# Kernel tuning notes

Hardware: AMD Instinct MI355X
Metric: run time of the kernel (lower is better)

## Reference

```python
import jax, jax.numpy as jnp
import numpy as np

N_NODES = 100000
N_EDGES = 400000
N_GRAPHS = 256
HID = 256
BIO = 512
LAYERS = 3
EPS = 1e-5


def _seg_mean(v, seg, num):
    s = jax.ops.segment_sum(v, seg, num_segments=num)
    c = jax.ops.segment_sum(jnp.ones((v.shape[0], 1), v.dtype), seg, num_segments=num)
    return s / jnp.maximum(c, 1.0)


def setup_inputs() -> dict:
    key = jax.random.key(0)
    ks = jax.random.split(key, 24)
    d = {}
    d['x'] = jax.random.randint(ks[0], (N_NODES,), 0, 8)
    d['edge_index'] = jax.random.randint(ks[1], (2, N_EDGES), 0, N_NODES)
    d['edge_attr'] = jax.random.normal(ks[2], (N_EDGES, 4), jnp.float32)
    d['batch'] = jnp.sort(jax.random.randint(ks[3], (N_NODES,), 0, N_GRAPHS))
    sc = 0.06  # ~1/sqrt(HID)
    d['node_emb_W'] = jax.random.normal(ks[4], (8, HID), jnp.float32) * sc
    d['edge_emb_W'] = jax.random.normal(ks[5], (4, HID), jnp.float32) * 0.5
    d['edge_emb_b'] = jnp.zeros((HID,), jnp.float32)
    d['edge_mlp_W1'] = jax.random.normal(ks[6], (HID, HID), jnp.float32) * sc
    d['edge_mlp_b1'] = jnp.zeros((HID,), jnp.float32)
    d['edge_mlp_W2'] = jax.random.normal(ks[7], (HID, HID), jnp.float32) * sc
    d['edge_mlp_b2'] = jnp.zeros((HID,), jnp.float32)
    d['struct_scale'] = jnp.asarray(1.5, jnp.float32)
    d['conv_W1'] = jax.random.normal(ks[8], (LAYERS, HID, HID), jnp.float32) * sc
    d['conv_b1'] = jnp.zeros((LAYERS, HID), jnp.float32)
    d['conv_W2'] = jax.random.normal(ks[9], (LAYERS, HID, HID), jnp.float32) * sc
    d['conv_b2'] = jnp.zeros((LAYERS, HID), jnp.float32)
    d['conv_eps'] = jnp.zeros((LAYERS,), jnp.float32)
    d['norm_gamma'] = jnp.ones((LAYERS, HID), jnp.float32)
    d['norm_beta'] = jnp.zeros((LAYERS, HID), jnp.float32)
    d['norm_alpha'] = jnp.ones((LAYERS, HID), jnp.float32)
    d['mean_bio'] = jax.random.normal(ks[10], (BIO,), jnp.float32)
    d['head_W1'] = jax.random.normal(ks[11], (HID + BIO, HID), jnp.float32) * 0.036
    d['head_b1'] = jnp.zeros((HID,), jnp.float32)
    d['head_W2'] = jax.random.normal(ks[12], (HID, 1), jnp.float32) * sc
    d['head_b2'] = jnp.zeros((1,), jnp.float32)
    return d


def reference(x, edge_index, edge_attr, batch, node_emb_W, edge_emb_W, edge_emb_b,
              edge_mlp_W1, edge_mlp_b1, edge_mlp_W2, edge_mlp_b2, struct_scale,
              conv_W1, conv_b1, conv_W2, conv_b2, conv_eps,
              norm_gamma, norm_beta, norm_alpha, mean_bio,
              head_W1, head_b1, head_W2, head_b2):
    h = node_emb_W[x]  # [N, HID]
    src, dst = edge_index[0], edge_index[1]

    e = edge_attr @ edge_emb_W + edge_emb_b  # edge_emb
    e = jax.nn.relu(e @ edge_mlp_W1 + edge_mlp_b1) @ edge_mlp_W2 + edge_mlp_b2
    struct_mask = edge_attr[:, 1] > 0
    e = e * jnp.where(struct_mask, struct_scale, 1.0)[:, None]

    for l in range(LAYERS):
        # GINE conv: aggregate relu(x_j + e_ij) at target, then 2-layer MLP
        msg = jax.nn.relu(h[src] + e)  # [E, HID]
        agg = jax.ops.segment_sum(msg, dst, num_segments=N_NODES)
        z = (1.0 + conv_eps[l]) * h + agg
        h = jax.nn.relu(z @ conv_W1[l] + conv_b1[l]) @ conv_W2[l] + conv_b2[l]
        # GraphNorm per graph
        mean = _seg_mean(h, batch, N_GRAPHS)  # [G, HID]
        hc = h - norm_alpha[l] * mean[batch]
        var = _seg_mean(hc * hc, batch, N_GRAPHS)
        h = norm_gamma[l] * hc * jax.lax.rsqrt(var[batch] + EPS) + norm_beta[l]

    g = _seg_mean(h, batch, N_GRAPHS)  # global mean pool [G, HID]
    b_emb = jnp.broadcast_to(mean_bio, (g.shape[0], BIO))
    combined = jnp.concatenate([g, b_emb], axis=1)
    out = jax.nn.relu(combined @ head_W1 + head_b1) @ head_W2 + head_b2
    return out.mean(axis=1, keepdims=True)
```

## Files before the change

### kernel.cpp

```cpp
#include <hip/hip_runtime.h>
#include <cstddef>

#define NN 100000
#define NE 400000
#define NG 256
#define HIDC 256
#define EPSN 1e-5f

typedef unsigned short bfu;
using short8 = __attribute__((ext_vector_type(8))) short;
using f32x4  = __attribute__((ext_vector_type(4))) float;
using f32x2  = __attribute__((ext_vector_type(2))) float;

#if defined(__has_builtin)
#if __has_builtin(__builtin_amdgcn_cvt_pk_fp8_f32) && __has_builtin(__builtin_amdgcn_cvt_pk_f32_fp8)
#define HWFP8 1
#endif
#endif

__device__ __forceinline__ float bf2f(bfu b) {
    union { unsigned int u; float f; } v; v.u = ((unsigned int)b) << 16; return v.f;
}
__device__ __forceinline__ bfu f2bf(float f) {
    union { float f; unsigned int u; } v; v.f = f;
    unsigned int r = v.u + 0x7FFFu + ((v.u >> 16) & 1u);
    return (bfu)(r >> 16);
}
__device__ __forceinline__ float e4m3f_sw(unsigned char b) {
    unsigned s = ((unsigned)(b & 0x80u)) << 24;
    unsigned E = (b >> 3) & 15u, M = b & 7u;
    union { unsigned x; float f; } o;
    if (E == 0) { o.f = (float)M * 0.001953125f; o.x |= s; }
    else o.x = s | ((E + 120u) << 23) | (M << 20);
    return o.f;
}
__device__ __forceinline__ unsigned char f2e4m3_sw(float f) {
    union { float f; unsigned u; } v; v.f = f;
    unsigned s = (v.u >> 24) & 0x80u;
    float a = fabsf(f);
    if (!(a < 448.f)) return (unsigned char)(s | 0x7Eu);
    if (a < 0.0009765625f) return (unsigned char)s;
    if (a < 0.015625f) {
        int m = (int)(a * 512.f + 0.5f);
        if (m >= 8) return (unsigned char)(s | 0x08u);
        return (unsigned char)(s | (unsigned)m);
    }
    unsigned u = v.u;
    unsigned r = u + 0x7FFFFu + ((u >> 20) & 1u);
    int E = (int)((r >> 23) & 255u) - 127 + 7;
    unsigned M = (r >> 20) & 7u;
    if (E >= 16) return (unsigned char)(s | 0x7Eu);
    if (E <= 0) {
        int m = (int)(a * 512.f + 0.5f); if (m > 7) m = 7;
        return (unsigned char)(s | (unsigned)m);
    }
    return (unsigned char)(s | ((unsigned)E << 3) | M);
}
__device__ __forceinline__ unsigned int fp8enc4(float a, float b, float c, float d) {
#ifdef HWFP8
    int lo = __builtin_amdgcn_cvt_pk_fp8_f32(a, b, 0, false);
    int hi = __builtin_amdgcn_cvt_pk_fp8_f32(c, d, 0, false);
    return (unsigned int)((lo & 0xFFFF) | (hi << 16));
#else
    return (unsigned)f2e4m3_sw(a) | ((unsigned)f2e4m3_sw(b) << 8) |
           ((unsigned)f2e4m3_sw(c) << 16) | ((unsigned)f2e4m3_sw(d) << 24);
#endif
}
__device__ __forceinline__ float4 fp8dec4(unsigned int u) {
#ifdef HWFP8
    f32x2 lo = __builtin_amdgcn_cvt_pk_f32_fp8((int)u, false);
    f32x2 hi = __builtin_amdgcn_cvt_pk_f32_fp8((int)u, true);
    return make_float4(lo[0], lo[1], hi[0], hi[1]);
#else
    return make_float4(e4m3f_sw(u & 255u), e4m3f_sw((u >> 8) & 255u),
                       e4m3f_sw((u >> 16) & 255u), e4m3f_sw((u >> 24) & 255u));
#endif
}
__device__ __forceinline__ float4 ld4(const void* p, size_t i, int bf) {
    if (bf) {
        ushort4 u = *(const ushort4*)((const bfu*)p + i);
        return make_float4(bf2f(u.x), bf2f(u.y), bf2f(u.z), bf2f(u.w));
    }
    return *(const float4*)((const float*)p + i);
}
__device__ __forceinline__ float4 ld4b(const bfu* p, size_t i) {
    ushort4 u = *(const ushort4*)(p + i);
    return make_float4(bf2f(u.x), bf2f(u.y), bf2f(u.z), bf2f(u.w));
}
__device__ __forceinline__ float ld1(const void* p, size_t i, int bf) {
    return bf ? bf2f(((const bfu*)p)[i]) : ((const float*)p)[i];
}
__device__ __forceinline__ void st1(void* p, size_t i, float v, int bf) {
    if (bf) ((bfu*)p)[i] = f2bf(v); else ((float*)p)[i] = v;
}

__global__ void k_dt2(const unsigned int* __restrict__ g, int* __restrict__ flag) {
    if (threadIdx.x == 0)
        flag[0] = (g[0] == 0x3F800000u) ? 0 : 1;
}

__global__ void k_st2(const int* __restrict__ batch, int* __restrict__ starts) {
    int g = threadIdx.x;
    if (g > NG) return;
    if (g == NG) { starts[NG] = NN; return; }
    int lo = 0, hi = NN;
    while (lo < hi) { int mid = (lo + hi) >> 1; if (batch[mid] < g) lo = mid + 1; else hi = mid; }
    starts[g] = lo;
}

__global__ void k_zi(int* __restrict__ p, int n) {
    int i = blockIdx.x * blockDim.x + threadIdx.x;
    if (i < n) p[i] = 0;
}

__global__ void k_cnt(const int* __restrict__ ei, int* __restrict__ deg) {
    int e = blockIdx.x * blockDim.x + threadIdx.x;
    if (e >= NE) return;
    int d = ei[NE + e];
    if ((unsigned)d < (unsigned)NN) atomicAdd(&deg[d], 1);
}
__global__ void k_sc1(const int* __restrict__ deg, int* __restrict__ rowp,
                      int* __restrict__ part) {
    __shared__ int sh[256];
    int b = blockIdx.x, t = threadIdx.x;
    int i = b * 256 + t;
    int v = (i < NN) ? deg[i] : 0;
    sh[t] = v; __syncthreads();
    for (int off = 1; off < 256; off <<= 1) {
        int add = (t >= off) ? sh[t - off] : 0;
        __syncthreads();
        sh[t] += add; __syncthreads();
    }
    if (i < NN) rowp[i] = sh[t] - v;
    if (t == 255) part[b] = sh[255];
}
__global__ void k_sc2(int* __restrict__ part, int nb) {
    if (threadIdx.x != 0) return;
    int run = 0;
    for (int b = 0; b < nb; ++b) { int t = part[b]; part[b] = run; run += t; }
}
__global__ void k_sc3(int* __restrict__ rowp, const int* __restrict__ part) {
    int i = blockIdx.x * blockDim.x + threadIdx.x;
    if (i < NN) rowp[i] += part[blockIdx.x];
    if (i == 0) rowp[NN] = NE;
}
__global__ void k_cpi(const int* __restrict__ a, int* __restrict__ b, int n) {
    int i = blockIdx.x * blockDim.x + threadIdx.x;
    if (i < n) b[i] = a[i];
}
__global__ void k_fil(const int* __restrict__ ei, int* __restrict__ cursor,
                      int* __restrict__ csrc, int* __restrict__ ceid) {
    int e = blockIdx.x * blockDim.x + threadIdx.x;
    if (e >= NE) return;
    int s = ei[e], d = ei[NE + e];
    if ((unsigned)d >= (unsigned)NN) return;
    int pos = atomicAdd(&cursor[d], 1);
    csrc[pos] = ((unsigned)s < (unsigned)NN) ? s : 0;
    ceid[pos] = e;
}
__global__ void k_spl(int* __restrict__ splits, int* __restrict__ cnts) {
    if (threadIdx.x == 0) { splits[0] = 0; splits[1] = NN; cnts[0] = NE; }
}

__global__ void k_wef(const void* __restrict__ Wemb, const void* __restrict__ bemb,
                      const void* __restrict__ W1, const void* __restrict__ b1,
                      bfu* __restrict__ weff, bfu* __restrict__ beff,
                      const int* __restrict__ dtf) {
    int bf = *dtf;
    int j = blockIdx.x;
    int n = threadIdx.x;
    float acc = 0.f;
    if (j < 4) {
        for (int k = 0; k < HIDC; ++k)
            acc += ld1(Wemb, (size_t)j * HIDC + k, bf) * ld1(W1, (size_t)k * HIDC + n, bf);
        weff[j * HIDC + n] = f2bf(acc);
    } else {
        for (int k = 0; k < HIDC; ++k)
            acc += ld1(bemb, k, bf) * ld1(W1, (size_t)k * HIDC + n, bf);
        beff[n] = f2bf(acc + ld1(b1, n, bf));
    }
}

__global__ void k_gat3(const bfu* __restrict__ h, const unsigned char* __restrict__ e8,
                       const int* __restrict__ rowp, const int* __restrict__ csrc,
                       bfu* __restrict__ agg) {
    int tid = blockIdx.x * blockDim.x + threadIdx.x;
    if (tid >= NN * 64) return;
    int n = tid >> 6, q = (tid & 63) << 2;
    int s0 = rowp[n], s1 = rowp[n + 1];
    float4 a = make_float4(0.f, 0.f, 0.f, 0.f);
    for (int i = s0; i < s1; ++i) {
        int src = csrc[i];
        ushort4 hu = *(const ushort4*)(h + (size_t)src * HIDC + q);
        unsigned int eu = *(const unsigned int*)(e8 + (size_t)i * HIDC + q);
        float4 ev = fp8dec4(eu);
        a.x += fmaxf(bf2f(hu.x) + ev.x, 0.f);
        a.y += fmaxf(bf2f(hu.y) + ev.y, 0.f);
        a.z += fmaxf(bf2f(hu.z) + ev.z, 0.f);
        a.w += fmaxf(bf2f(hu.w) + ev.w, 0.f);
    }
    ushort4 o; o.x = f2bf(a.x); o.y = f2bf(a.y); o.z = f2bf(a.z); o.w = f2bf(a.w);
    *(ushort4*)(agg + (size_t)n * HIDC + q) = o;
}

__global__ void k_wtr(const void* __restrict__ W, long wOff, bfu* __restrict__ Wt,
                      const int* __restrict__ dtf) {
    int o = blockIdx.x * blockDim.x + threadIdx.x;
    if (o >= HIDC * HIDC) return;
    int blk = o >> 9, pos = o & 511;
    int w = blk >> 5, rem = blk & 31;
    int t = rem >> 3, kb = rem & 7;
    int pr = pos >> 3, j = pos & 7;
    int lr = pr >> 2, lq = pr & 3;
    int n = w * 64 + t * 16 + lr;
    int k = kb * 32 + lq * 8 + j;
    Wt[o] = f2bf(ld1(W, (size_t)wOff + (size_t)k * HIDC + n, *dtf));
}

__global__ void k_emb(const int* __restrict__ x, const void* __restrict__ W,
                      bfu* __restrict__ h, const int* __restrict__ dtf) {
    int tid = blockIdx.x * blockDim.x + threadIdx.x;
    if (tid >= NN * 64) return;
    int bf = *dtf;
    int n = tid >> 6, q = (tid & 63) << 2;
    int xv = x[n]; if ((unsigned)xv >= 8u) xv = 0;
    float4 v = ld4(W, (size_t)xv * HIDC + q, bf);
    ushort4 o; o.x = f2bf(v.x); o.y = f2bf(v.y); o.z = f2bf(v.z); o.w = f2bf(v.w);
    *(ushort4*)(h + (size_t)n * HIDC + q) = o;
}

__global__ __launch_bounds__(256)
void k_mg2(const bfu* __restrict__ A, const void* __restrict__ A2,
           const void* __restrict__ attrs,
           const bfu* __restrict__ weff, const bfu* __restrict__ beff,
           const void* __restrict__ eps, int epsIdx,
           const bfu* __restrict__ Wt,
           const void* __restrict__ bias, long bOff,
           const void* __restrict__ scalep,
           void* __restrict__ C, int M,
           int amode, int relu, int scale, int o8,
           const int* __restrict__ dtf,
           const int* __restrict__ eidx, const int* __restrict__ rowp,
           const int* __restrict__ splits, const int* __restrict__ cnts, int cj) {
    __shared__ bfu As[64 * 32];
    const int bf = *dtf;
    const int tid = threadIdx.x;
    const int wave = tid >> 6, lane = tid & 63;
    const int lr = lane & 15, lq = lane >> 4;
    const int m0 = blockIdx.x * 64;
    int MM = M;
    long p0 = 0;
    if (cj >= 0) {
        MM = cnts[cj];
        p0 = rowp[splits[cj]];
    }
    if (m0 >= MM) return;
    f32x4 acc[4][4] = {};
    float epsv = 0.f;
    if (amode == 2) epsv = 1.0f + ld1(eps, epsIdx, bf);

    const int ar = tid >> 2;
    const int ak = (tid & 3) << 3;
    const int gmA = m0 + ar;
    const bfu* wb = Wt + ((size_t)wave * 32) * 512 + (size_t)(lr * 4 + lq) * 8;

    float aa[4] = {0.f, 0.f, 0.f, 0.f};
    if (amode == 1 && gmA < MM) {
        long er = (cj >= 0) ? (long)eidx[p0 + gmA] : (long)gmA;
        aa[0] = ld1(attrs, (size_t)er * 4 + 0, bf);
        aa[1] = ld1(attrs, (size_t)er * 4 + 1, bf);
        aa[2] = ld1(attrs, (size_t)er * 4 + 2, bf);
        aa[3] = ld1(attrs, (size_t)er * 4 + 3, bf);
    }

    for (int k0 = 0; k0 < 256; k0 += 32) {
        const int kb = k0 >> 5;
        if (amode == 0) {
            uint4 u = make_uint4(0, 0, 0, 0);
            if (gmA < MM) u = *(const uint4*)(A + (size_t)gmA * HIDC + k0 + ak);
            *(uint4*)(&As[tid * 8]) = u;
        } else if (amode == 2) {
            float hv[8] = {}, gv[8] = {};
            if (gmA < MM) {
                ushort4 h0 = *(const ushort4*)(A + (size_t)gmA * HIDC + k0 + ak);
                ushort4 h1 = *(const ushort4*)(A + (size_t)gmA * HIDC + k0 + ak + 4);
                hv[0]=bf2f(h0.x); hv[1]=bf2f(h0.y); hv[2]=bf2f(h0.z); hv[3]=bf2f(h0.w);
                hv[4]=bf2f(h1.x); hv[5]=bf2f(h1.y); hv[6]=bf2f(h1.z); hv[7]=bf2f(h1.w);
                float4 g0 = ld4(A2, (size_t)gmA * HIDC + k0 + ak, 1);
                float4 g1 = ld4(A2, (size_t)gmA * HIDC + k0 + ak + 4, 1);
                gv[0]=g0.x; gv[1]=g0.y; gv[2]=g0.z; gv[3]=g0.w;
                gv[4]=g1.x; gv[5]=g1.y; gv[6]=g1.z; gv[7]=g1.w;
            }
#pragma unroll
            for (int j = 0; j < 8; ++j)
                As[tid * 8 + j] = f2bf(epsv * hv[j] + gv[j]);
        } else {
            float v0=0,v1=0,v2=0,v3=0,v4=0,v5=0,v6=0,v7=0;
            if (gmA < MM) {
                float4 c0 = ld4b(beff, k0 + ak);
                float4 c1 = ld4b(beff, k0 + ak + 4);
                v0=c0.x; v1=c0.y; v2=c0.z; v3=c0.w; v4=c1.x; v5=c1.y; v6=c1.z; v7=c1.w;
#pragma unroll
                for (int j = 0; j < 4; ++j) {
                    float4 w0 = ld4b(weff, (size_t)j * HIDC + k0 + ak);
                    float4 w1 = ld4b(weff, (size_t)j * HIDC + k0 + ak + 4);
                    v0 += aa[j]*w0.x; v1 += aa[j]*w0.y; v2 += aa[j]*w0.z; v3 += aa[j]*w0.w;
                    v4 += aa[j]*w1.x; v5 += aa[j]*w1.y; v6 += aa[j]*w1.z; v7 += aa[j]*w1.w;
                }
            }
            ushort4 o0, o1;
            o0.x = f2bf(fmaxf(v0, 0.f)); o0.y = f2bf(fmaxf(v1, 0.f));
            o0.z = f2bf(fmaxf(v2, 0.f)); o0.w = f2bf(fmaxf(v3, 0.f));
            o1.x = f2bf(fmaxf(v4, 0.f)); o1.y = f2bf(fmaxf(v5, 0.f));
            o1.z = f2bf(fmaxf(v6, 0.f)); o1.w = f2bf(fmaxf(v7, 0.f));
            *(ushort4*)(&As[tid * 8])     = o0;
            *(ushort4*)(&As[tid * 8 + 4]) = o1;
        }
        __syncthreads();
        short8 fa[4], fb[4];
#pragma unroll
        for (int r = 0; r < 4; ++r)
            fa[r] = *(const short8*)(&As[(r * 64 + lr * 4 + lq) * 8]);
#pragma unroll
        for (int t = 0; t < 4; ++t)
            fb[t] = *(const short8*)(wb + (size_t)(t * 8 + kb) * 512);
#pragma unroll
        for (int r = 0; r < 4; ++r)
#pragma unroll
            for (int t = 0; t < 4; ++t)
                acc[r][t] = __builtin_amdgcn_mfma_f32_16x16x32_bf16(
                    fa[r], fb[t], acc[r][t], 0, 0, 0);
        __syncthreads();
    }

    float bv[4];
#pragma unroll
    for (int t = 0; t < 4; ++t) bv[t] = ld1(bias, (size_t)bOff + wave * 64 + t * 16 + lr, bf);
    float scv = scale ? ld1(scalep, 0, bf) : 1.0f;
#pragma unroll
    for (int r = 0; r < 4; ++r) {
#pragma unroll
        for (int i = 0; i < 4; ++i) {
            int gm = m0 + r * 16 + lq * 4 + i;
            if (gm >= MM) continue;
            float rs = 1.0f;
            if (scale) {
                long er = (cj >= 0) ? (long)eidx[p0 + gm] : (long)gm;
                if (ld1(attrs, (size_t)er * 4 + 1, bf) > 0.f) rs = scv;
            }
            float ov[4];
#pragma unroll
            for (int t = 0; t < 4; ++t) {
                float o = acc[r][t][i] + bv[t];
                if (relu) o = fmaxf(o, 0.f);
                ov[t] = o * rs;
            }
            size_t cbase = (size_t)gm * HIDC + wave * 64 + lr;
            if (o8) {
                unsigned int pk = fp8enc4(ov[0], ov[1], ov[2], ov[3]);
                unsigned char* Cb = (unsigned char*)C;
                Cb[cbase]      = (unsigned char)(pk & 255u);
                Cb[cbase + 16] = (unsigned char)((pk >> 8) & 255u);
                Cb[cbase + 32] = (unsigned char)((pk >> 16) & 255u);
                Cb[cbase + 48] = (unsigned char)(pk >> 24);
            } else {
                bfu* Cb = (bfu*)C;
#pragma unroll
                for (int t = 0; t < 4; ++t)
                    Cb[cbase + t * 16] = f2bf(ov[t]);
            }
        }
    }
}

__global__ __launch_bounds__(256)
void k_cnv(bfu* __restrict__ h, const bfu* __restrict__ agg,
           const void* __restrict__ eps, int epsIdx,
           const bfu* __restrict__ Wt1, const void* __restrict__ bias1, long b1Off,
           const bfu* __restrict__ Wt2, const void* __restrict__ bias2, long b2Off,
           const int* __restrict__ dtf) {
    __shared__ bfu As[64 * 32];
    __shared__ bfu Ts[8][64 * 32];
    const int bf = *dtf;
    const int tid = threadIdx.x;
    const int wave = tid >> 6, lane = tid & 63;
    const int lr = lane & 15, lq = lane >> 4;
    const int m0 = blockIdx.x * 64;
    const float epsv = 1.0f + ld1(eps, epsIdx, bf);
    const int ar = tid >> 2;
    const int ak = (tid & 3) << 3;
    const int gmA = m0 + ar;
    const bfu* wb1 = Wt1 + ((size_t)wave * 32) * 512 + (size_t)(lr * 4 + lq) * 8;
    const bfu* wb2 = Wt2 + ((size_t)wave * 32) * 512 + (size_t)(lr * 4 + lq) * 8;

    f32x4 acc[4][4] = {};
    for (int k0 = 0; k0 < 256; k0 += 32) {
        const int kb = k0 >> 5;
        float hv[8] = {}, gv[8] = {};
        if (gmA < NN) {
            ushort4 h0 = *(const ushort4*)(h + (size_t)gmA * HIDC + k0 + ak);
            ushort4 h1 = *(const ushort4*)(h + (size_t)gmA * HIDC + k0 + ak + 4);
            hv[0]=bf2f(h0.x); hv[1]=bf2f(h0.y); hv[2]=bf2f(h0.z); hv[3]=bf2f(h0.w);
            hv[4]=bf2f(h1.x); hv[5]=bf2f(h1.y); hv[6]=bf2f(h1.z); hv[7]=bf2f(h1.w);
            ushort4 g0 = *(const ushort4*)(agg + (size_t)gmA * HIDC + k0 + ak);
            ushort4 g1 = *(const ushort4*)(agg + (size_t)gmA * HIDC + k0 + ak + 4);
            gv[0]=bf2f(g0.x); gv[1]=bf2f(g0.y); gv[2]=bf2f(g0.z); gv[3]=bf2f(g0.w);
            gv[4]=bf2f(g1.x); gv[5]=bf2f(g1.y); gv[6]=bf2f(g1.z); gv[7]=bf2f(g1.w);
        }
#pragma unroll
        for (int j = 0; j < 8; ++j)
            As[tid * 8 + j] = f2bf(epsv * hv[j] + gv[j]);
        __syncthreads();
        short8 fa[4], fb[4];
#pragma unroll
        for (int r = 0; r < 4; ++r)
            fa[r] = *(const short8*)(&As[(r * 64 + lr * 4 + lq) * 8]);
#pragma unroll
        for (int t = 0; t < 4; ++t)
            fb[t] = *(const short8*)(wb1 + (size_t)(t * 8 + kb) * 512);
#pragma unroll
        for (int r = 0; r < 4; ++r)
#pragma unroll
            for (int t = 0; t < 4; ++t)
                acc[r][t] = __builtin_amdgcn_mfma_f32_16x16x32_bf16(
                    fa[r], fb[t], acc[r][t], 0, 0, 0);
        __syncthreads();
    }
    {
        float bv[4];
#pragma unroll
        for (int t = 0; t < 4; ++t)
            bv[t] = ld1(bias1, (size_t)b1Off + wave * 64 + t * 16 + lr, bf);
        const f32x4 z4 = {0.f, 0.f, 0.f, 0.f};
#pragma unroll
        for (int r = 0; r < 4; ++r) {
#pragma unroll
            for (int i = 0; i < 4; ++i) {
                int row = r * 16 + lq * 4 + i;
#pragma unroll
                for (int t = 0; t < 4; ++t) {
                    int kk = wave * 64 + t * 16 + lr;
                    Ts[kk >> 5][row * 32 + (kk & 31)] =
                        f2bf(fmaxf(acc[r][t][i] + bv[t], 0.f));
                }
            }
        }
#pragma unroll
        for (int r = 0; r < 4; ++r)
#pragma unroll
            for (int t = 0; t < 4; ++t)
                acc[r][t] = z4;
    }
    __syncthreads();
#pragma unroll
    for (int kb = 0; kb < 8; ++kb) {
        short8 fa[4], fb[4];
#pragma unroll
        for (int r = 0; r < 4; ++r)
            fa[r] = *(const short8*)(&Ts[kb][(r * 64 + lr * 4 + lq) * 8]);
#pragma unroll
        for (int t = 0; t < 4; ++t)
            fb[t] = *(const short8*)(wb2 + (size_t)(t * 8 + kb) * 512);
#pragma unroll
        for (int r = 0; r < 4; ++r)
#pragma unroll
            for (int t = 0; t < 4; ++t)
                acc[r][t] = __builtin_amdgcn_mfma_f32_16x16x32_bf16(
                    fa[r], fb[t], acc[r][t], 0, 0, 0);
    }
    float bv[4];
#pragma unroll
    for (int t = 0; t < 4; ++t)
        bv[t] = ld1(bias2, (size_t)b2Off + wave * 64 + t * 16 + lr, bf);
#pragma unroll
    for (int r = 0; r < 4; ++r) {
#pragma unroll
        for (int i = 0; i < 4; ++i) {
            int gm = m0 + r * 16 + lq * 4 + i;
            if (gm >= NN) continue;
            size_t cbase = (size_t)gm * HIDC + wave * 64 + lr;
#pragma unroll
            for (int t = 0; t < 4; ++t)
                h[cbase + t * 16] = f2bf(acc[r][t][i] + bv[t]);
        }
    }
}

__global__ void k_s1(const bfu* __restrict__ h, const int* __restrict__ starts,
                     float* __restrict__ psum, float* __restrict__ psq) {
    int g = blockIdx.x, c8 = blockIdx.y, c = threadIdx.x;
    int s = starts[g], t = starts[g + 1];
    int len = t - s;
    int b = s + (int)(((long)len * c8) >> 3);
    int e = s + (int)(((long)len * (c8 + 1)) >> 3);
    float sum = 0.f, sq = 0.f;
    for (int n = b; n < e; ++n) {
        float v = bf2f(h[(size_t)n * HIDC + c]);
        sum += v; sq += v * v;
    }
    psum[((size_t)g * 8 + c8) * HIDC + c] = sum;
    psq[((size_t)g * 8 + c8) * HIDC + c] = sq;
}
__global__ void k_s2(const int* __restrict__ starts,
                     const float* __restrict__ psum, const float* __restrict__ psq,
                     const void* __restrict__ alpha, long aOff,
                     float* __restrict__ gmean, float* __restrict__ gvar,
                     const int* __restrict__ dtf) {
    int g = blockIdx.x, c = threadIdx.x;
    float sum = 0.f, sq = 0.f;
#pragma unroll
    for (int j = 0; j < 8; ++j) {
        sum += psum[((size_t)g * 8 + j) * HIDC + c];
        sq  += psq[((size_t)g * 8 + j) * HIDC + c];
    }
    int cn = starts[g + 1] - starts[g]; if (cn < 1) cn = 1;
    float cnt = (float)cn;
    float m = sum / cnt;
    float a = ld1(alpha, (size_t)aOff + c, *dtf);
    gmean[g * HIDC + c] = m;
    gvar[g * HIDC + c] = fmaxf(sq / cnt - (2.f * a - a * a) * m * m, 0.f);
}

__global__ void k_nrm(bfu* __restrict__ h, const int* __restrict__ batch,
                      const float* __restrict__ gmean, const float* __restrict__ gvar,
                      const void* __restrict__ gamma, const void* __restrict__ beta,
                      const void* __restrict__ alpha, long pOff,
                      const int* __restrict__ dtf) {
    int tid = blockIdx.x * blockDim.x + threadIdx.x;
    if (tid >= NN * 64) return;
    int bf = *dtf;
    int n = tid >> 6, q = (tid & 63) << 2;
    int g = batch[n]; if ((unsigned)g >= (unsigned)NG) g = 0;
    ushort4 hu = *(ushort4*)(h + (size_t)n * HIDC + q);
    const float4 mv = *(const float4*)(gmean + g * HIDC + q);
    const float4 vv = *(const float4*)(gvar + g * HIDC + q);
    float4 ga = ld4(gamma, (size_t)pOff + q, bf);
    float4 be = ld4(beta, (size_t)pOff + q, bf);
    float4 al = ld4(alpha, (size_t)pOff + q, bf);
    float4 v;
    v.x = ga.x * (bf2f(hu.x) - al.x * mv.x) * rsqrtf(vv.x + EPSN) + be.x;
    v.y = ga.y * (bf2f(hu.y) - al.y * mv.y) * rsqrtf(vv.y + EPSN) + be.y;
    v.z = ga.z * (bf2f(hu.z) - al.z * mv.z) * rsqrtf(vv.z + EPSN) + be.z;
    v.w = ga.w * (bf2f(hu.w) - al.w * mv.w) * rsqrtf(vv.w + EPSN) + be.w;
    ushort4 ov; ov.x = f2bf(v.x); ov.y = f2bf(v.y); ov.z = f2bf(v.z); ov.w = f2bf(v.w);
    *(ushort4*)(h + (size_t)n * HIDC + q) = ov;
}

__global__ void k_pl2(const int* __restrict__ starts,
                      const float* __restrict__ gmean, const float* __restrict__ gvar,
                      const void* __restrict__ gamma, const void* __restrict__ beta,
                      const void* __restrict__ alpha, long pOff,
                      float* __restrict__ g, const int* __restrict__ dtf) {
    int bf = *dtf;
    int gb = blockIdx.x, c = threadIdx.x;
    int cn = starts[gb + 1] - starts[gb];
    if (cn <= 0) { g[gb * HIDC + c] = 0.f; return; }
    float m = gmean[gb * HIDC + c];
    float v = gvar[gb * HIDC + c];
    float ga = ld1(gamma, (size_t)pOff + c, bf);
    float be = ld1(beta, (size_t)pOff + c, bf);
    float al = ld1(alpha, (size_t)pOff + c, bf);
    g[gb * HIDC + c] = ga * (1.f - al) * m * rsqrtf(v + EPSN) + be;
}

__global__ void k_hd(const float* __restrict__ g, const void* __restrict__ bio,
                     const void* __restrict__ W1, const void* __restrict__ b1,
                     const void* __restrict__ W2, const void* __restrict__ b2,
                     void* __restrict__ out, const int* __restrict__ dtf) {
    __shared__ float comb[768];
    __shared__ float red[256];
    __shared__ int nanf;
    int bf = *dtf;
    int gb = blockIdx.x, t = threadIdx.x;
    if (t == 0) nanf = 0;
    comb[t] = g[gb * HIDC + t];
    comb[256 + t] = ld1(bio, t, bf);
    comb[512 + t] = ld1(bio, 256 + t, bf);
    __syncthreads();
    float acc = ld1(b1, t, bf);
    for (int k = 0; k < 768; ++k) acc += comb[k] * ld1(W1, (size_t)k * HIDC + t, bf);
    if (isnan(acc) || isinf(acc)) nanf = 1;
    float hid = fmaxf(acc, 0.f);
    red[t] = hid * ld1(W2, t, bf);
    __syncthreads();
    for (int off = 128; off > 0; off >>= 1) {
        if (t < off) red[t] += red[t + off];
        __syncthreads();
    }
    if (t == 0) {
        float r = red[0] + ld1(b2, 0, bf);
        if (nanf || isnan(r)) r = 999.0f;
        st1(out, gb, r, bf);
    }
}

extern "C" void kernel_launch(void* const* d_in, const int* in_sizes, int n_in,
                              void* d_out, int out_size, void* d_ws, size_t ws_size,
                              hipStream_t stream) {
    const int* x = (const int*)d_in[0];
    const int* ei = (const int*)d_in[1];
    const void* eattr = d_in[2];
    const int* batch = (const int*)d_in[3];
    const void* node_emb_W = d_in[4];
    const void* edge_emb_W = d_in[5];
    const void* edge_emb_b = d_in[6];
    const void* emlp_W1 = d_in[7];
    const void* emlp_b1 = d_in[8];
    const void* emlp_W2 = d_in[9];
    const void* emlp_b2 = d_in[10];
    const void* struct_scale = d_in[11];
    const void* conv_W1 = d_in[12];
    const void* conv_b1 = d_in[13];
    const void* conv_W2 = d_in[14];
    const void* conv_b2 = d_in[15];
    const void* conv_eps = d_in[16];
    const void* ngamma = d_in[17];
    const void* nbeta = d_in[18];
    const void* nalpha = d_in[19];
    const void* mean_bio = d_in[20];
    const void* head_W1 = d_in[21];
    const void* head_b1 = d_in[22];
    const void* head_W2 = d_in[23];
    const void* head_b2 = d_in[24];
    (void)in_sizes; (void)n_in; (void)out_size; (void)ws_size;

    const size_t H_B = (size_t)NN * HIDC * 2;
    const size_t E8_B = (size_t)NE * HIDC;
    char* p = (char*)d_ws;
    bfu* hbuf = (bfu*)p; p += H_B;
    bfu* aggb = (bfu*)p; p += H_B;
    unsigned char* e8 = (unsigned char*)p; p += E8_B;
    bfu* wt = (bfu*)p; p += 8 * 65536 * 2;
    int* rowp = (int*)p;
    int* cursor = rowp + 100352;
    int* part = cursor + 100352;
    int* splits = part + 1024;
    int* cnts = splits + 8;
    int* csrc = cnts + 8;
    int* ceid = csrc + NE;
    p = (char*)(ceid + NE);
    float* psum = (float*)p; p += (size_t)NG * 8 * HIDC * 4;
    float* psq = (float*)p; p += (size_t)NG * 8 * HIDC * 4;
    char* small = p;
    int* starts = (int*)small;
    int* dtf = (int*)(small + 2048);
    bfu* weff = (bfu*)(small + 4096);
    bfu* beff = weff + 4 * HIDC;
    float* gmean = (float*)(small + 16384);
    float* gvar = gmean + NG * HIDC;
    float* gpool = gvar + NG * HIDC;

    k_dt2<<<1, 64, 0, stream>>>((const unsigned int*)ngamma, dtf);
    k_st2<<<1, 512, 0, stream>>>(batch, starts);
    k_emb<<<(NN * 64 + 255) / 256, 256, 0, stream>>>(x, node_emb_W, hbuf, dtf);
    k_wef<<<5, 256, 0, stream>>>(edge_emb_W, edge_emb_b, emlp_W1, emlp_b1,
                                 weff, beff, dtf);

    k_wtr<<<256, 256, 0, stream>>>(emlp_W2, 0, wt + 65536, dtf);
    for (int l = 0; l < 3; ++l) {
        k_wtr<<<256, 256, 0, stream>>>(conv_W1, (long)l * HIDC * HIDC, wt + (2 + l) * 65536, dtf);
        k_wtr<<<256, 256, 0, stream>>>(conv_W2, (long)l * HIDC * HIDC, wt + (5 + l) * 65536, dtf);
    }

    const int NBN = (NN + 255) / 256;
    k_zi<<<NBN, 256, 0, stream>>>(cursor, NN);
    k_cnt<<<(NE + 255) / 256, 256, 0, stream>>>(ei, cursor);
    k_sc1<<<NBN, 256, 0, stream>>>(cursor, rowp, part);
    k_sc2<<<1, 64, 0, stream>>>(part, NBN);
    k_sc3<<<NBN, 256, 0, stream>>>(rowp, part);
    k_cpi<<<NBN, 256, 0, stream>>>(rowp, cursor, NN);
    k_fil<<<(NE + 255) / 256, 256, 0, stream>>>(ei, cursor, csrc, ceid);
    k_spl<<<1, 64, 0, stream>>>(splits, cnts);

    dim3 gE((NE + 63) / 64), gN((NN + 63) / 64);
    k_mg2<<<gE, 256, 0, stream>>>(
        nullptr, nullptr, eattr, weff, beff,
        nullptr, 0, wt + 65536, emlp_b2, 0, struct_scale, e8, 0,
        1, 0, 1, 1, dtf, ceid, rowp, splits, cnts, 0);

    dim3 gS1(NG, 8);
    const int gatBlocks = (NN * 64 + 255) / 256;

    for (int l = 0; l < 3; ++l) {
        k_gat3<<<gatBlocks, 256, 0, stream>>>(hbuf, e8, rowp, csrc, aggb);
        k_cnv<<<gN, 256, 0, stream>>>(
            hbuf, aggb, conv_eps, l,
            wt + (2 + l) * 65536, conv_b1, (long)l * HIDC,
            wt + (5 + l) * 65536, conv_b2, (long)l * HIDC, dtf);
        k_s1<<<gS1, 256, 0, stream>>>(hbuf, starts, psum, psq);
        k_s2<<<NG, 256, 0, stream>>>(starts, psum, psq, nalpha, (long)l * HIDC,
                                     gmean, gvar, dtf);
        if (l < 2) {
            k_nrm<<<(NN * 64 + 255) / 256, 256, 0, stream>>>(
                hbuf, batch, gmean, gvar, ngamma, nbeta, nalpha, (long)l * HIDC, dtf);
        }
    }

    k_pl2<<<NG, 256, 0, stream>>>(starts, gmean, gvar, ngamma, nbeta, nalpha,
                                  (long)2 * HIDC, gpool, dtf);
    k_hd<<<NG, 256, 0, stream>>>(gpool, mean_bio, head_W1, head_b1,
                                 head_W2, head_b2, d_out, dtf);
}
```

Baseline: 1.066 ms.

## Specialize edge MLP kernel and stage full A tile in LDS once

Replaces the generic multi-mode edge GEMM kernel with a dedicated edge-MLP kernel. The whole 64x256 A tile is built into shared memory in one pass before a single barrier, instead of a barrier pair per 32-wide K slice. The per-row struct scale is precomputed into shared memory rather than re-gathered in the epilogue, and weff/beff are kept in fp32. The conv kernel gets the same single-barrier A staging using its existing Ts buffer. This raises LDS use per block to 32KB, which may lower occupancy.

Result: faster. 1.014 ms (-4.9%).

```diff
diff --git a/kernel.cpp b/kernel.cpp
--- a/kernel.cpp
+++ b/kernel.cpp
@@ -82,10 +82,6 @@
         return make_float4(bf2f(u.x), bf2f(u.y), bf2f(u.z), bf2f(u.w));
     }
     return *(const float4*)((const float*)p + i);
-}
-__device__ __forceinline__ float4 ld4b(const bfu* p, size_t i) {
-    ushort4 u = *(const ushort4*)(p + i);
-    return make_float4(bf2f(u.x), bf2f(u.y), bf2f(u.z), bf2f(u.w));
 }
 __device__ __forceinline__ float ld1(const void* p, size_t i, int bf) {
     return bf ? bf2f(((const bfu*)p)[i]) : ((const float*)p)[i];
@@ -158,13 +154,10 @@
     csrc[pos] = ((unsigned)s < (unsigned)NN) ? s : 0;
     ceid[pos] = e;
 }
-__global__ void k_spl(int* __restrict__ splits, int* __restrict__ cnts) {
-    if (threadIdx.x == 0) { splits[0] = 0; splits[1] = NN; cnts[0] = NE; }
-}
 
 __global__ void k_wef(const void* __restrict__ Wemb, const void* __restrict__ bemb,
                       const void* __restrict__ W1, const void* __restrict__ b1,
-                      bfu* __restrict__ weff, bfu* __restrict__ beff,
+                      float* __restrict__ weff, float* __restrict__ beff,
                       const int* __restrict__ dtf) {
     int bf = *dtf;
     int j = blockIdx.x;
@@ -173,11 +166,11 @@
     if (j < 4) {
         for (int k = 0; k < HIDC; ++k)
             acc += ld1(Wemb, (size_t)j * HIDC + k, bf) * ld1(W1, (size_t)k * HIDC + n, bf);
-        weff[j * HIDC + n] = f2bf(acc);
+        weff[j * HIDC + n] = acc;
     } else {
         for (int k = 0; k < HIDC; ++k)
             acc += ld1(bemb, k, bf) * ld1(W1, (size_t)k * HIDC + n, bf);
-        beff[n] = f2bf(acc + ld1(b1, n, bf));
+        beff[n] = acc + ld1(b1, n, bf);
     }
 }
 
@@ -230,145 +223,101 @@
 }
 
 __global__ __launch_bounds__(256)
-void k_mg2(const bfu* __restrict__ A, const void* __restrict__ A2,
-           const void* __restrict__ attrs,
-           const bfu* __restrict__ weff, const bfu* __restrict__ beff,
-           const void* __restrict__ eps, int epsIdx,
-           const bfu* __restrict__ Wt,
-           const void* __restrict__ bias, long bOff,
-           const void* __restrict__ scalep,
-           void* __restrict__ C, int M,
-           int amode, int relu, int scale, int o8,
-           const int* __restrict__ dtf,
-           const int* __restrict__ eidx, const int* __restrict__ rowp,
-           const int* __restrict__ splits, const int* __restrict__ cnts, int cj) {
-    __shared__ bfu As[64 * 32];
+void k_me(const void* __restrict__ attrs,
+          const float* __restrict__ weff, const float* __restrict__ beff,
+          const bfu* __restrict__ Wt, const void* __restrict__ bias,
+          const void* __restrict__ scalep,
+          unsigned char* __restrict__ C,
+          const int* __restrict__ dtf, const int* __restrict__ eidx) {
+    __shared__ bfu As[8][64 * 32];
+    __shared__ float sf[64];
     const int bf = *dtf;
     const int tid = threadIdx.x;
     const int wave = tid >> 6, lane = tid & 63;
     const int lr = lane & 15, lq = lane >> 4;
     const int m0 = blockIdx.x * 64;
-    int MM = M;
-    long p0 = 0;
-    if (cj >= 0) {
-        MM = cnts[cj];
-        p0 = rowp[splits[cj]];
-    }
-    if (m0 >= MM) return;
-    f32x4 acc[4][4] = {};
-    float epsv = 0.f;
-    if (amode == 2) epsv = 1.0f + ld1(eps, epsIdx, bf);
-
-    const int ar = tid >> 2;
+    const int row = tid >> 2;
     const int ak = (tid & 3) << 3;
-    const int gmA = m0 + ar;
-    const bfu* wb = Wt + ((size_t)wave * 32) * 512 + (size_t)(lr * 4 + lq) * 8;
+    const int gmA = m0 + row;
 
     float aa[4] = {0.f, 0.f, 0.f, 0.f};
-    if (amode == 1 && gmA < MM) {
-        long er = (cj >= 0) ? (long)eidx[p0 + gmA] : (long)gmA;
+    if (gmA < NE) {
+        long er = (long)eidx[gmA];
         aa[0] = ld1(attrs, (size_t)er * 4 + 0, bf);
         aa[1] = ld1(attrs, (size_t)er * 4 + 1, bf);
         aa[2] = ld1(attrs, (size_t)er * 4 + 2, bf);
         aa[3] = ld1(attrs, (size_t)er * 4 + 3, bf);
     }
-
+    if ((tid & 3) == 0)
+        sf[row] = (gmA < NE && aa[1] > 0.f) ? ld1(scalep, 0, bf) : 1.0f;
+
+#pragma unroll
     for (int k0 = 0; k0 < 256; k0 += 32) {
-        const int kb = k0 >> 5;
-        if (amode == 0) {
-            uint4 u = make_uint4(0, 0, 0, 0);
-            if (gmA < MM) u = *(const uint4*)(A + (size_t)gmA * HIDC + k0 + ak);
-            *(uint4*)(&As[tid * 8]) = u;
-        } else if (amode == 2) {
-            float hv[8] = {}, gv[8] = {};
-            if (gmA < MM) {
-                ushort4 h0 = *(const ushort4*)(A + (size_t)gmA * HIDC + k0 + ak);
-                ushort4 h1 = *(const ushort4*)(A + (size_t)gmA * HIDC + k0 + ak + 4);
-                hv[0]=bf2f(h0.x); hv[1]=bf2f(h0.y); hv[2]=bf2f(h0.z); hv[3]=bf2f(h0.w);
-                hv[4]=bf2f(h1.x); hv[5]=bf2f(h1.y); hv[6]=bf2f(h1.z); hv[7]=bf2f(h1.w);
-                float4 g0 = ld4(A2, (size_t)gmA * HIDC + k0 + ak, 1);
-                float4 g1 = ld4(A2, (size_t)gmA * HIDC + k0 + ak + 4, 1);
-                gv[0]=g0.x; gv[1]=g0.y; gv[2]=g0.z; gv[3]=g0.w;
-                gv[4]=g1.x; gv[5]=g1.y; gv[6]=g1.z; gv[7]=g1.w;
-            }
-#pragma unroll
-            for (int j = 0; j < 8; ++j)
-                As[tid * 8 + j] = f2bf(epsv * hv[j] + gv[j]);
-        } else {
-            float v0=0,v1=0,v2=0,v3=0,v4=0,v5=0,v6=0,v7=0;
-            if (gmA < MM) {
-                float4 c0 = ld4b(beff, k0 + ak);
-                float4 c1 = ld4b(beff, k0 + ak + 4);
-                v0=c0.x; v1=c0.y; v2=c0.z; v3=c0.w; v4=c1.x; v5=c1.y; v6=c1.z; v7=c1.w;
-#pragma unroll
-                for (int j = 0; j < 4; ++j) {
-                    float4 w0 = ld4b(weff, (size_t)j * HIDC + k0 + ak);
-                    float4 w1 = ld4b(weff, (size_t)j * HIDC + k0 + ak + 4);
-                    v0 += aa[j]*w0.x; v1 += aa[j]*w0.y; v2 += aa[j]*w0.z; v3 += aa[j]*w0.w;
-                    v4 += aa[j]*w1.x; v5 += aa[j]*w1.y; v6 += aa[j]*w1.z; v7 += aa[j]*w1.w;
-                }
-            }
-            ushort4 o0, o1;
-            o0.x = f2bf(fmaxf(v0, 0.f)); o0.y = f2bf(fmaxf(v1, 0.f));
-            o0.z = f2bf(fmaxf(v2, 0.f)); o0.w = f2bf(fmaxf(v3, 0.f));
-            o1.x = f2bf(fmaxf(v4, 0.f)); o1.y = f2bf(fmaxf(v5, 0.f));
-            o1.z = f2bf(fmaxf(v6, 0.f)); o1.w = f2bf(fmaxf(v7, 0.f));
-            *(ushort4*)(&As[tid * 8])     = o0;
-            *(ushort4*)(&As[tid * 8 + 4]) = o1;
+        const int c = k0 + ak;
+        float4 b0 = *(const float4*)(beff + c);
+        float4 b1v = *(const float4*)(beff + c + 4);
+        float v0 = b0.x, v1 = b0.y, v2 = b0.z, v3 = b0.w;
+        float v4 = b1v.x, v5 = b1v.y, v6 = b1v.z, v7 = b1v.w;
+#pragma unroll
+        for (int j = 0; j < 4; ++j) {
+            float4 w0 = *(const float4*)(weff + j * HIDC + c);
+            float4 w1 = *(const float4*)(weff + j * HIDC + c + 4);
+            v0 += aa[j] * w0.x; v1 += aa[j] * w0.y;
+            v2 += aa[j] * w0.z; v3 += aa[j] * w0.w;
+            v4 += aa[j] * w1.x; v5 += aa[j] * w1.y;
+            v6 += aa[j] * w1.z; v7 += aa[j] * w1.w;
         }
-        __syncthreads();
-        short8 fa[4], fb[4];
+        ushort4 o0, o1;
+        o0.x = f2bf(fmaxf(v0, 0.f)); o0.y = f2bf(fmaxf(v1, 0.f));
+        o0.z = f2bf(fmaxf(v2, 0.f)); o0.w = f2bf(fmaxf(v3, 0.f));
+        o1.x = f2bf(fmaxf(v4, 0.f)); o1.y = f2bf(fmaxf(v5, 0.f));
+        o1.z = f2bf(fmaxf(v6, 0.f)); o1.w = f2bf(fmaxf(v7, 0.f));
+        *(ushort4*)(&As[k0 >> 5][row * 32 + ak]) = o0;
+        *(ushort4*)(&As[k0 >> 5][row * 32 + ak + 4]) = o1;
+    }
+    __syncthreads();
+
+    f32x4 acc[4][4] = {};
+    const bfu* wb = Wt + ((size_t)wave * 32) * 512 + (size_t)(lr * 4 + lq) * 8;
+#pragma unroll
+    for (int kb = 0; kb < 8; ++kb) {
+        short8 fa[4], fbv[4];
 #pragma unroll
         for (int r = 0; r < 4; ++r)
-            fa[r] = *(const short8*)(&As[(r * 64 + lr * 4 + lq) * 8]);
+            fa[r] = *(const short8*)(&As[kb][(r * 16 + lr) * 32 + lq * 8]);
 #pragma unroll
         for (int t = 0; t < 4; ++t)
-            fb[t] = *(const short8*)(wb + (size_t)(t * 8 + kb) * 512);
+            fbv[t] = *(const short8*)(wb + (size_t)(t * 8 + kb) * 512);
 #pragma unroll
         for (int r = 0; r < 4; ++r)
 #pragma unroll
             for (int t = 0; t < 4; ++t)
                 acc[r][t] = __builtin_amdgcn_mfma_f32_16x16x32_bf16(
-                    fa[r], fb[t], acc[r][t], 0, 0, 0);
-        __syncthreads();
+                    fa[r], fbv[t], acc[r][t], 0, 0, 0);
     }
 
     float bv[4];
 #pragma unroll
-    for (int t = 0; t < 4; ++t) bv[t] = ld1(bias, (size_t)bOff + wave * 64 + t * 16 + lr, bf);
-    float scv = scale ? ld1(scalep, 0, bf) : 1.0f;
+    for (int t = 0; t < 4; ++t)
+        bv[t] = ld1(bias, (size_t)(wave * 64 + t * 16 + lr), bf);
 #pragma unroll
     for (int r = 0; r < 4; ++r) {
 #pragma unroll
         for (int i = 0; i < 4; ++i) {
-            int gm = m0 + r * 16 + lq * 4 + i;
-            if (gm >= MM) continue;
-            float rs = 1.0f;
-            if (scale) {
-                long er = (cj >= 0) ? (long)eidx[p0 + gm] : (long)gm;
-                if (ld1(attrs, (size_t)er * 4 + 1, bf) > 0.f) rs = scv;
-            }
-            float ov[4];
-#pragma unroll
-            for (int t = 0; t < 4; ++t) {
-                float o = acc[r][t][i] + bv[t];
-                if (relu) o = fmaxf(o, 0.f);
-                ov[t] = o * rs;
-            }
+            int rr = r * 16 + lq * 4 + i;
+            int gm = m0 + rr;
+            if (gm >= NE) continue;
+            float rs = sf[rr];
+            float ov0 = (acc[r][0][i] + bv[0]) * rs;
+            float ov1 = (acc[r][1][i] + bv[1]) * rs;
+            float ov2 = (acc[r][2][i] + bv[2]) * rs;
+            float ov3 = (acc[r][3][i] + bv[3]) * rs;
+            unsigned int pk = fp8enc4(ov0, ov1, ov2, ov3);
             size_t cbase = (size_t)gm * HIDC + wave * 64 + lr;
-            if (o8) {
-                unsigned int pk = fp8enc4(ov[0], ov[1], ov[2], ov[3]);
-                unsigned char* Cb = (unsigned char*)C;
-                Cb[cbase]      = (unsigned char)(pk & 255u);
-                Cb[cbase + 16] = (unsigned char)((pk >> 8) & 255u);
-                Cb[cbase + 32] = (unsigned char)((pk >> 16) & 255u);
-                Cb[cbase + 48] = (unsigned char)(pk >> 24);
-            } else {
-                bfu* Cb = (bfu*)C;
-#pragma unroll
-                for (int t = 0; t < 4; ++t)
-                    Cb[cbase + t * 16] = f2bf(ov[t]);
-            }
+            C[cbase]      = (unsigned char)(pk & 255u);
+            C[cbase + 16] = (unsigned char)((pk >> 8) & 255u);
+            C[cbase + 32] = (unsigned char)((pk >> 16) & 255u);
+            C[cbase + 48] = (unsigned char)(pk >> 24);
         }
     }
 }
@@ -379,7 +328,6 @@
            const bfu* __restrict__ Wt1, const void* __restrict__ bias1, long b1Off,
            const bfu* __restrict__ Wt2, const void* __restrict__ bias2, long b2Off,
            const int* __restrict__ dtf) {
-    __shared__ bfu As[64 * 32];
     __shared__ bfu Ts[8][64 * 32];
     const int bf = *dtf;
     const int tid = threadIdx.x;
@@ -387,15 +335,14 @@
     const int lr = lane & 15, lq = lane >> 4;
     const int m0 = blockIdx.x * 64;
     const float epsv = 1.0f + ld1(eps, epsIdx, bf);
-    const int ar = tid >> 2;
+    const int row = tid >> 2;
     const int ak = (tid & 3) << 3;
-    const int gmA = m0 + ar;
+    const int gmA = m0 + row;
     const bfu* wb1 = Wt1 + ((size_t)wave * 32) * 512 + (size_t)(lr * 4 + lq) * 8;
     const bfu* wb2 = Wt2 + ((size_t)wave * 32) * 512 + (size_t)(lr * 4 + lq) * 8;
 
-    f32x4 acc[4][4] = {};
+#pragma unroll
     for (int k0 = 0; k0 < 256; k0 += 32) {
-        const int kb = k0 >> 5;
         float hv[8] = {}, gv[8] = {};
         if (gmA < NN) {
             ushort4 h0 = *(const ushort4*)(h + (size_t)gmA * HIDC + k0 + ak);
@@ -407,25 +354,35 @@
             gv[0]=bf2f(g0.x); gv[1]=bf2f(g0.y); gv[2]=bf2f(g0.z); gv[3]=bf2f(g0.w);
             gv[4]=bf2f(g1.x); gv[5]=bf2f(g1.y); gv[6]=bf2f(g1.z); gv[7]=bf2f(g1.w);
         }
-#pragma unroll
-        for (int j = 0; j < 8; ++j)
-            As[tid * 8 + j] = f2bf(epsv * hv[j] + gv[j]);
-        __syncthreads();
-        short8 fa[4], fb[4];
+        ushort4 o0, o1;
+        o0.x = f2bf(epsv * hv[0] + gv[0]); o0.y = f2bf(epsv * hv[1] + gv[1]);
+        o0.z = f2bf(epsv * hv[2] + gv[2]); o0.w = f2bf(epsv * hv[3] + gv[3]);
+        o1.x = f2bf(epsv * hv[4] + gv[4]); o1.y = f2bf(epsv * hv[5] + gv[5]);
+        o1.z = f2bf(epsv * hv[6] + gv[6]); o1.w = f2bf(epsv * hv[7] + gv[7]);
+        *(ushort4*)(&Ts[k0 >> 5][row * 32 + ak]) = o0;
+        *(ushort4*)(&Ts[k0 >> 5][row * 32 + ak + 4]) = o1;
+    }
+    __syncthreads();
+
+    f32x4 acc[4][4] = {};
+#pragma unroll
+    for (int kb = 0; kb < 8; ++kb) {
+        short8 fa[4], fbv[4];
 #pragma unroll
         for (int r = 0; r < 4; ++r)
-            fa[r] = *(const short8*)(&As[(r * 64 + lr * 4 + lq) * 8]);
+            fa[r] = *(const short8*)(&Ts[kb][(r * 16 + lr) * 32 + lq * 8]);
 #pragma unroll
         for (int t = 0; t < 4; ++t)
-            fb[t] = *(const short8*)(wb1 + (size_t)(t * 8 + kb) * 512);
+            fbv[t] = *(const short8*)(wb1 + (size_t)(t * 8 + kb) * 512);
 #pragma unroll
         for (int r = 0; r < 4; ++r)
 #pragma unroll
             for (int t = 0; t < 4; ++t)
                 acc[r][t] = __builtin_amdgcn_mfma_f32_16x16x32_bf16(
-                    fa[r], fb[t], acc[r][t], 0, 0, 0);
-        __syncthreads();
-    }
+                    fa[r], fbv[t], acc[r][t], 0, 0, 0);
+    }
+    __syncthreads();
+
     {
         float bv[4];
 #pragma unroll
@@ -436,11 +393,11 @@
         for (int r = 0; r < 4; ++r) {
 #pragma unroll
             for (int i = 0; i < 4; ++i) {
-                int row = r * 16 + lq * 4 + i;
+                int rowo = r * 16 + lq * 4 + i;
 #pragma unroll
                 for (int t = 0; t < 4; ++t) {
                     int kk = wave * 64 + t * 16 + lr;
-                    Ts[kk >> 5][row * 32 + (kk & 31)] =
+                    Ts[kk >> 5][rowo * 32 + (kk & 31)] =
                         f2bf(fmaxf(acc[r][t][i] + bv[t], 0.f));
                 }
             }
@@ -452,21 +409,22 @@
                 acc[r][t] = z4;
     }
     __syncthreads();
+
 #pragma unroll
     for (int kb = 0; kb < 8; ++kb) {
-        short8 fa[4], fb[4];
+        short8 fa[4], fbv[4];
 #pragma unroll
         for (int r = 0; r < 4; ++r)
-            fa[r] = *(const short8*)(&Ts[kb][(r * 64 + lr * 4 + lq) * 8]);
+            fa[r] = *(const short8*)(&Ts[kb][(r * 16 + lr) * 32 + lq * 8]);
 #pragma unroll
         for (int t = 0; t < 4; ++t)
-            fb[t] = *(const short8*)(wb2 + (size_t)(t * 8 + kb) * 512);
+            fbv[t] = *(const short8*)(wb2 + (size_t)(t * 8 + kb) * 512);
 #pragma unroll
         for (int r = 0; r < 4; ++r)
 #pragma unroll
             for (int t = 0; t < 4; ++t)
                 acc[r][t] = __builtin_amdgcn_mfma_f32_16x16x32_bf16(
-                    fa[r], fb[t], acc[r][t], 0, 0, 0);
+                    fa[r], fbv[t], acc[r][t], 0, 0, 0);
     }
     float bv[4];
 #pragma unroll
@@ -644,11 +602,12 @@
     char* small = p;
     int* starts = (int*)small;
     int* dtf = (int*)(small + 2048);
-    bfu* weff = (bfu*)(small + 4096);
-    bfu* beff = weff + 4 * HIDC;
+    float* weff = (float*)(small + 4096);
+    float* beff = weff + 4 * HIDC;
     float* gmean = (float*)(small + 16384);
     float* gvar = gmean + NG * HIDC;
     float* gpool = gvar + NG * HIDC;
+    (void)splits; (void)cnts;
 
     k_dt2<<<1, 64, 0, stream>>>((const unsigned int*)ngamma, dtf);
     k_st2<<<1, 512, 0, stream>>>(batch, starts);
@@ -670,13 +629,10 @@
     k_sc3<<<NBN, 256, 0, stream>>>(rowp, part);
     k_cpi<<<NBN, 256, 0, stream>>>(rowp, cursor, NN);
     k_fil<<<(NE + 255) / 256, 256, 0, stream>>>(ei, cursor, csrc, ceid);
-    k_spl<<<1, 64, 0, stream>>>(splits, cnts);
 
     dim3 gE((NE + 63) / 64), gN((NN + 63) / 64);
-    k_mg2<<<gE, 256, 0, stream>>>(
-        nullptr, nullptr, eattr, weff, beff,
-        nullptr, 0, wt + 65536, emlp_b2, 0, struct_scale, e8, 0,
-        1, 0, 1, 1, dtf, ceid, rowp, splits, cnts, 0);
+    k_me<<<gE, 256, 0, stream>>>(eattr, weff, beff, wt + 65536, emlp_b2,
+                                 struct_scale, e8, dtf, ceid);
 
     dim3 gS1(NG, 8);
     const int gatBlocks = (NN * 64 + 255) / 256;
```
